# Optimization experiments

Measured on AMD Instinct MI355X. Metric: run time of the kernel, lower is better.

The kernel has to match this reference:

```python
import jax, jax.numpy as jnp
import numpy as np

B, IN_DIM, C, E, TOPK = 16384, 768, 50, 8, 2
RH = 256          # router hidden_dim
HS = [512, 256]   # expert hidden_sizes
THR = 0.05        # BitNet-1.58b ternarization threshold


def _xavier(k, shape):
    fan_out, fan_in = shape[-2], shape[-1]
    lim = float(np.sqrt(6.0 / (fan_in + fan_out)))
    return jax.random.uniform(k, shape, jnp.float32, -lim, lim)


def setup_inputs() -> dict:
    key = jax.random.key(0)
    ks = jax.random.split(key, 8)
    return {
        "x": jax.random.normal(ks[0], (B, IN_DIM), jnp.float32),
        # Router MLP: in_dim -> RH -> RH//2 -> E (torch Linear: W is (out,in))
        "rW1": _xavier(ks[1], (RH, IN_DIM)), "rb1": jnp.zeros((RH,), jnp.float32),
        "rW2": _xavier(ks[2], (RH // 2, RH)), "rb2": jnp.zeros((RH // 2,), jnp.float32),
        "rW3": _xavier(ks[3], (E, RH // 2)), "rb3": jnp.zeros((E,), jnp.float32),
        # Stacked expert weights: (E, out, in)
        "eW1": _xavier(ks[4], (E, HS[0], IN_DIM)), "eb1": jnp.zeros((E, HS[0]), jnp.float32),
        "eW2": _xavier(ks[5], (E, HS[1], HS[0])), "eb2": jnp.zeros((E, HS[1]), jnp.float32),
        "eW3": _xavier(ks[6], (E, C, HS[1])), "eb3": jnp.zeros((E, C), jnp.float32),
    }


def _ternary(W):
    # BitNet-1.58b: ternarize weights with |w|>threshold, scale by mean |W| per matrix
    scale = jnp.mean(jnp.abs(W), axis=(-2, -1), keepdims=True)
    Wq = jnp.sign(W) * (jnp.abs(W) > THR).astype(W.dtype)
    return Wq * scale


def reference(x, rW1, rb1, rW2, rb2, rW3, rb3, eW1, eb1, eW2, eb2, eW3, eb3):
    # ---- Router (eval mode: dropout = identity) ----
    h = jax.nn.relu(x @ rW1.T + rb1)
    h = jax.nn.relu(h @ rW2.T + rb2)
    router_logits = h @ rW3.T + rb3                      # (B, E)
    router_p = jax.nn.softmax(router_logits, axis=1)     # (B, E)

    # ---- Top-k gating; scatter gate weights back to dense (B, E) ----
    k_val, k_idx = jax.lax.top_k(router_p, TOPK)         # (B, K)
    rows = jnp.arange(x.shape[0])[:, None]
    gate = jnp.zeros_like(router_p).at[rows, k_idx].set(k_val)  # 0 for unselected experts

    # ---- Batched ternary-quantized expert MLPs (all experts, all samples) ----
    W1q, W2q, W3q = _ternary(eW1), _ternary(eW2), _ternary(eW3)
    a1 = jax.nn.relu(jnp.einsum('bd,ehd->ebh', x, W1q) + eb1[:, None, :])   # (E,B,H1)
    a2 = jax.nn.relu(jnp.einsum('ebh,egh->ebg', a1, W2q) + eb2[:, None, :]) # (E,B,H2)
    expert_logits = jnp.einsum('ebg,ecg->ebc', a2, W3q) + eb3[:, None, :]   # (E,B,C)

    # ---- Weighted combine over top-k experts (equivalent to the per-expert loop) ----
    out = jnp.einsum('ebc,be->bc', expert_logits, gate) / TOPK              # (B,C)

    lb_loss = jnp.float32(0.0)  # eval mode: self.training is False
    return (out, router_p, lb_loss)
```

## Files before the change

### kernel.cpp

```cpp
#include <hip/hip_runtime.h>
#include <hip/hip_bf16.h>

typedef __attribute__((ext_vector_type(4))) float f32x4;
typedef __attribute__((ext_vector_type(8))) short bf16x8;

#define B_ROWS 16384
#define IN_DIM 768
#define H1 512
#define H2 256
#define NC 50
#define NE 8
#define RH1 256
#define RH2 128
#define CHK 128
#define CHKX 64

static __device__ __forceinline__ f32x4 mfma16(bf16x8 a, bf16x8 b, f32x4 c) {
    return __builtin_amdgcn_mfma_f32_16x16x32_bf16(a, b, c, 0, 0, 0);
}

typedef __attribute__((address_space(1))) const unsigned int gas_u32;
typedef __attribute__((address_space(3))) unsigned int las_u32;
static __device__ __forceinline__ void gl16(const void* g, void* l) {
    __builtin_amdgcn_global_load_lds((gas_u32*)g, (las_u32*)l, 16, 0, 0);
}

static __device__ __forceinline__ bf16x8 expand_frag(uint2 pw) {
    unsigned q0 = (pw.x & 0x01010101u) << 7;
    unsigned q1 = (pw.y & 0x01010101u) << 7;
    union { unsigned u[4]; bf16x8 v; } r;
    r.u[0] = __builtin_amdgcn_perm(pw.x, q0, 0x05010400u);
    r.u[1] = __builtin_amdgcn_perm(pw.x, q0, 0x07030602u);
    r.u[2] = __builtin_amdgcn_perm(pw.y, q1, 0x05010400u);
    r.u[3] = __builtin_amdgcn_perm(pw.y, q1, 0x07030602u);
    return r.v;
}

static __device__ __forceinline__ void decomp_f4(float4 v, ushort4* hv, ushort4* lv) {
    float vv[4] = {v.x, v.y, v.z, v.w};
    ushort ho[4], lo4[4];
    #pragma unroll
    for (int q = 0; q < 4; ++q) {
        __hip_bfloat16 h = __float2bfloat16(vv[q]);
        float hf = __bfloat162float(h);
        __hip_bfloat16 l = __float2bfloat16(vv[q] - hf);
        ho[q] = *(ushort*)&h; lo4[q] = *(ushort*)&l;
    }
    *hv = make_ushort4(ho[0], ho[1], ho[2], ho[3]);
    *lv = make_ushort4(lo4[0], lo4[1], lo4[2], lo4[3]);
}

static __device__ __forceinline__ ushort4 cvt_f4_bf16(float4 v) {
    float vv[4] = {v.x, v.y, v.z, v.w};
    ushort ho[4];
    #pragma unroll
    for (int q = 0; q < 4; ++q) {
        __hip_bfloat16 h = __float2bfloat16(vv[q]);
        ho[q] = *(ushort*)&h;
    }
    return make_ushort4(ho[0], ho[1], ho[2], ho[3]);
}

__global__ __launch_bounds__(512) void pack_absum_kernel(
    const float* __restrict__ eW1, const float* __restrict__ eW2, const float* __restrict__ eW3,
    unsigned char* __restrict__ W1p8, unsigned char* __restrict__ W2p8,
    unsigned char* __restrict__ W3p8,
    float* __restrict__ p1, float* __restrict__ p2, float* __restrict__ p3)
{
    const int mat = blockIdx.y >> 3, e = blockIdx.y & 7;
    const int u = blockIdx.x * 512 + threadIdx.x;
    const float* src; unsigned char* dst; int valid = 1; float* P; int np;
    if (mat == 0) {
        int lane = u & 63, nblk = (u >> 6) & 31, ks = u >> 11;
        int n = nblk * 16 + (lane & 15), k = ks * 32 + (lane >> 4) * 8;
        src = eW1 + ((size_t)e * H1 + n) * IN_DIM + k;
        dst = W1p8 + (size_t)e * 393216
            + (size_t)ks * 16384 + (nblk >> 1) * 1024 + lane * 16 + (nblk & 1) * 8;
        P = p1; np = 96;
    } else if (mat == 1) {
        if (u >= 16384) return;
        int lane = u & 63, nblk = (u >> 6) & 15, ks = u >> 10;
        int n = nblk * 16 + (lane & 15), k = ks * 32 + (lane >> 4) * 8;
        src = eW2 + ((size_t)e * H2 + n) * H1 + k;
        dst = W2p8 + (size_t)e * 131072
            + (size_t)ks * 8192 + (nblk >> 1) * 1024 + lane * 16 + (nblk & 1) * 8;
        P = p2; np = 32;
    } else {
        if (u >= 2048) return;
        int lane = u & 63, nblk = (u >> 6) & 3, ks = u >> 8;
        int n = nblk * 16 + (lane & 15), k = ks * 32 + (lane >> 4) * 8;
        valid = (n < NC);
        src = eW3 + ((size_t)e * NC + (valid ? n : 0)) * H2 + k;
        dst = W3p8 + ((size_t)e * 2048 + u) * 8;
        P = p3; np = 4;
    }
    unsigned lo = 0, hi = 0;
    float s = 0.f;
    #pragma unroll
    for (int j = 0; j < 4; ++j) {
        float w = valid ? src[j] : 0.f;
        s += fabsf(w);
        unsigned c = (fabsf(w) > 0.05f) ? (w > 0.f ? 0x3Fu : 0xBFu) : 0u;
        lo |= c << (8 * j);
    }
    #pragma unroll
    for (int j = 0; j < 4; ++j) {
        float w = valid ? src[4 + j] : 0.f;
        s += fabsf(w);
        unsigned c = (fabsf(w) > 0.05f) ? (w > 0.f ? 0x3Fu : 0xBFu) : 0u;
        hi |= c << (8 * j);
    }
    *(uint2*)dst = make_uint2(lo, hi);
    const int lane = threadIdx.x & 63, wave = threadIdx.x >> 6;
    #pragma unroll
    for (int o = 32; o; o >>= 1) s += __shfl_down(s, o);
    __shared__ float red[8];
    if (lane == 0) red[wave] = s;
    __syncthreads();
    if (threadIdx.x == 0) {
        float t = 0.f;
        #pragma unroll
        for (int i = 0; i < 8; ++i) t += red[i];
        P[e * np + blockIdx.x] = t;
    }
}

__global__ __launch_bounds__(64) void finalize_scales_kernel(
    const float* __restrict__ p1, const float* __restrict__ p2, const float* __restrict__ p3,
    float* __restrict__ s1, float* __restrict__ s2, float* __restrict__ s3,
    int* __restrict__ counts)
{
    int t = threadIdx.x;
    if (t < 8) {
        float a = 0.f;
        for (int i = 0; i < 96; ++i) a += p1[t * 96 + i];
        s1[t] = a / (float)(H1 * IN_DIM);
    } else if (t < 16) {
        int e = t - 8; float a = 0.f;
        for (int i = 0; i < 32; ++i) a += p2[e * 32 + i];
        s2[e] = a / (float)(H2 * H1);
    } else if (t < 24) {
        int e = t - 16; float a = 0.f;
        for (int i = 0; i < 4; ++i) a += p3[e * 4 + i];
        s3[e] = a / (float)(NC * H2);
    } else if (t < 32) {
        counts[t - 24] = 0;
    }
}

__global__ __launch_bounds__(512) void pack_router_kernel(
    const float* __restrict__ rW1, ushort* __restrict__ rw1hp, ushort* __restrict__ rw1lp,
    const float* __restrict__ rW2, ushort* __restrict__ rw2hp, ushort* __restrict__ rw2lp)
{
    int u = blockIdx.x * 512 + threadIdx.x;
    const float* src; ushort* dh; ushort* dl;
    if (u < 24576) {
        int lane = u & 63, nblk = (u >> 6) & 15, ks = u >> 10;
        int n = nblk * 16 + (lane & 15), k = ks * 32 + (lane >> 4) * 8;
        src = rW1 + (size_t)n * IN_DIM + k;
        dh = rw1hp + (size_t)u * 8; dl = rw1lp + (size_t)u * 8;
    } else {
        int v = u - 24576;
        if (v >= 4096) return;
        int lane = v & 63, nblk = (v >> 6) & 7, ks = v >> 9;
        int n = nblk * 16 + (lane & 15), k = ks * 32 + (lane >> 4) * 8;
        src = rW2 + (size_t)n * RH1 + k;
        dh = rw2hp + (size_t)v * 8; dl = rw2lp + (size_t)v * 8;
    }
    ushort oh[8], ol[8];
    #pragma unroll
    for (int j = 0; j < 8; ++j) {
        float w = src[j];
        __hip_bfloat16 h = __float2bfloat16(w);
        float hf = __bfloat162float(h);
        __hip_bfloat16 l = __float2bfloat16(w - hf);
        oh[j] = *(ushort*)&h; ol[j] = *(ushort*)&l;
    }
    ((ushort4*)dh)[0] = make_ushort4(oh[0], oh[1], oh[2], oh[3]);
    ((ushort4*)dh)[1] = make_ushort4(oh[4], oh[5], oh[6], oh[7]);
    ((ushort4*)dl)[0] = make_ushort4(ol[0], ol[1], ol[2], ol[3]);
    ((ushort4*)dl)[1] = make_ushort4(ol[4], ol[5], ol[6], ol[7]);
}

__global__ __launch_bounds__(1024) void router_fused_kernel(
    const float* __restrict__ x,
    const ushort* __restrict__ rw1hp, const ushort* __restrict__ rw1lp, const float* __restrict__ rb1,
    const ushort* __restrict__ rw2hp, const ushort* __restrict__ rw2lp, const float* __restrict__ rb2,
    const float* __restrict__ rW3, const float* __restrict__ rb3,
    float* __restrict__ router_p, float* __restrict__ gate,
    float* __restrict__ lb_out, int* __restrict__ t2)
{
    __shared__ __align__(16) unsigned char smem[134144];
    unsigned char* Wst = smem;
    ushort (*Xdh)[32][136] = (ushort(*)[32][136])(smem + 65536);
    ushort (*Xdl)[32][136] = (ushort(*)[32][136])(smem + 65536 + 17408);
    float (*h2s)[132]      = (float(*)[132])(smem + 65536);
    ushort (*h1hs)[264]    = (ushort(*)[264])(smem + 100352);
    ushort (*h1ls)[264]    = (ushort(*)[264])(smem + 117248);

    const int tid = threadIdx.x, wave = tid >> 6, lane = tid & 63;
    const int lm = lane & 15, lk = lane >> 4;
    const int r0 = blockIdx.x * 32;

    const int srow = tid >> 5;
    const int sc4r = (tid & 31) * 4;
    const float* sg = x + (size_t)(r0 + srow) * IN_DIM + sc4r;

    float4 sv = *(const float4*)sg;
    gl16(rw1hp + tid * 8, Wst + tid * 16);
    gl16(rw1lp + tid * 8, Wst + 16384 + tid * 16);
    {
        ushort4 hv, lv;
        decomp_f4(sv, &hv, &lv);
        *(ushort4*)&Xdh[0][srow][sc4r] = hv;
        *(ushort4*)&Xdl[0][srow][sc4r] = lv;
    }
    __syncthreads();

    {
        f32x4 acc[2] = {};
        for (int s = 0; s < 24; ++s) {
            const int c = s >> 2;
            const unsigned char* curh = Wst + (s & 1) * 32768;
            const unsigned char* curl = curh + 16384;
            if (s + 1 < 24) {
                unsigned char* dst = Wst + ((s + 1) & 1) * 32768;
                gl16(rw1hp + (size_t)(s + 1) * 8192 + tid * 8, dst + tid * 16);
                gl16(rw1lp + (size_t)(s + 1) * 8192 + tid * 8, dst + 16384 + tid * 16);
            } else {
                if (tid < 512) gl16(rw2hp + tid * 8, Wst + tid * 16);
                else           gl16(rw2lp + (tid & 511) * 8, Wst + 16384 + (tid & 511) * 16);
            }
            if ((s & 3) == 0 && c < 5)
                sv = *(const float4*)(sg + (c + 1) * CHK);
            const ushort (*Xch)[136] = Xdh[c & 1];
            const ushort (*Xcl)[136] = Xdl[c & 1];
            const int ko = (s & 3) * 32 + lk * 8;
            bf16x8 ah0 = *(const bf16x8*)&Xch[lm][ko];
            bf16x8 al0 = *(const bf16x8*)&Xcl[lm][ko];
            bf16x8 ah1 = *(const bf16x8*)&Xch[16 + lm][ko];
            bf16x8 al1 = *(const bf16x8*)&Xcl[16 + lm][ko];
            bf16x8 bh = *(const bf16x8*)(curh + (wave * 64 + lane) * 16);
            bf16x8 bl = *(const bf16x8*)(curl + (wave * 64 + lane) * 16);
            acc[0] = mfma16(ah0, bh, acc[0]);
            acc[0] = mfma16(ah0, bl, acc[0]);
            acc[0] = mfma16(al0, bh, acc[0]);
            acc[1] = mfma16(ah1, bh, acc[1]);
            acc[1] = mfma16(ah1, bl, acc[1]);
            acc[1] = mfma16(al1, bh, acc[1]);
            if ((s & 3) == 2 && c < 5) {
                ushort4 hv, lv;
                decomp_f4(sv, &hv, &lv);
                *(ushort4*)&Xdh[(c + 1) & 1][srow][sc4r] = hv;
                *(ushort4*)&Xdl[(c + 1) & 1][srow][sc4r] = lv;
            }
            __syncthreads();
        }
        int col = wave * 16 + lm;
        float bv = rb1[col];
        #pragma unroll
        for (int m = 0; m < 2; ++m)
            #pragma unroll
            for (int r = 0; r < 4; ++r) {
                float v = acc[m][r] + bv;
                v = v > 0.f ? v : 0.f;
                __hip_bfloat16 h = __float2bfloat16(v);
                float hf = __bfloat162float(h);
                __hip_bfloat16 l = __float2bfloat16(v - hf);
                int row = m * 16 + lk * 4 + r;
                h1hs[row][col] = *(ushort*)&h;
                h1ls[row][col] = *(ushort*)&l;
            }
    }
    __syncthreads();

    {
        const int mt = wave >> 3, nb = wave & 7;
        f32x4 acc2 = {};
        for (int s = 0; s < 8; ++s) {
            const unsigned char* curh = Wst + (s & 1) * 32768;
            const unsigned char* curl = curh + 16384;
            if (s + 1 < 8) {
                unsigned char* dst = Wst + ((s + 1) & 1) * 32768;
                if (tid < 512) gl16(rw2hp + (size_t)(s + 1) * 4096 + tid * 8, dst + tid * 16);
                else           gl16(rw2lp + (size_t)(s + 1) * 4096 + (tid & 511) * 8, dst + 16384 + (tid & 511) * 16);
            }
            const int ko = s * 32 + lk * 8;
            bf16x8 ah = *(const bf16x8*)&h1hs[mt * 16 + lm][ko];
            bf16x8 al = *(const bf16x8*)&h1ls[mt * 16 + lm][ko];
            bf16x8 bh = *(const bf16x8*)(curh + (nb * 64 + lane) * 16);
            bf16x8 bl = *(const bf16x8*)(curl + (nb * 64 + lane) * 16);
            acc2 = mfma16(ah, bh, acc2);
            acc2 = mfma16(ah, bl, acc2);
            acc2 = mfma16(al, bh, acc2);
            __syncthreads();
        }
        int col2 = nb * 16 + lm;
        float bv = rb2[col2];
        #pragma unroll
        for (int r = 0; r < 4; ++r) {
            float v = acc2[r] + bv;
            h2s[mt * 16 + lk * 4 + r][col2] = v > 0.f ? v : 0.f;
        }
    }
    __syncthreads();

    const int o = lane >> 3, kq = lane & 7;
    #pragma unroll
    for (int i = 0; i < 2; ++i) {
        int rloc = wave * 2 + i;
        int b = r0 + rloc;
        float s = 0.f;
        #pragma unroll
        for (int q = 0; q < 4; ++q) {
            float4 hv = *(const float4*)&h2s[rloc][kq * 16 + q * 4];
            float4 wv = *(const float4*)&rW3[o * RH2 + kq * 16 + q * 4];
            s += hv.x * wv.x + hv.y * wv.y + hv.z * wv.z + hv.w * wv.w;
        }
        s += __shfl_xor(s, 1);
        s += __shfl_xor(s, 2);
        s += __shfl_xor(s, 4);
        float logit = s + rb3[o];
        float l[8];
        #pragma unroll
        for (int j = 0; j < 8; ++j) l[j] = __shfl(logit, j * 8);
        float m = l[0];
        #pragma unroll
        for (int j = 1; j < 8; ++j) m = fmaxf(m, l[j]);
        float p[8]; float sum = 0.f;
        #pragma unroll
        for (int j = 0; j < 8; ++j) { p[j] = expf(l[j] - m); sum += p[j]; }
        float inv = 1.f / sum;
        #pragma unroll
        for (int j = 0; j < 8; ++j) p[j] *= inv;
        int i1 = 0; float v1 = p[0];
        #pragma unroll
        for (int j = 1; j < 8; ++j) if (p[j] > v1) { v1 = p[j]; i1 = j; }
        int i2 = -1; float v2 = -1.f;
        #pragma unroll
        for (int j = 0; j < 8; ++j) if (j != i1 && p[j] > v2) { v2 = p[j]; i2 = j; }
        if (lane < 8) {
            router_p[(size_t)b * 8 + lane] = p[lane];
            float gv = (lane == i1) ? v1 * 0.5f : ((lane == i2) ? v2 * 0.5f : 0.f);
            gate[(size_t)b * 8 + lane] = gv;
        }
        if (lane == 0) t2[b] = i1 | (i2 << 8);
    }
    if (blockIdx.x == 0 && tid == 0) lb_out[0] = 0.f;
}

__global__ __launch_bounds__(256) void build_lists_kernel(
    const int* __restrict__ t2, int* __restrict__ counts, int* __restrict__ ent)
{
    __shared__ int hist[8], base[8];
    const int r = blockIdx.x * 256 + threadIdx.x;
    if (threadIdx.x < 8) hist[threadIdx.x] = 0;
    __syncthreads();
    const int v = t2[r];
    const int i1 = v & 255, i2 = v >> 8;
    const int rk1 = atomicAdd(&hist[i1], 1);
    const int rk2 = atomicAdd(&hist[i2], 1);
    __syncthreads();
    if (threadIdx.x < 8) base[threadIdx.x] = atomicAdd(&counts[threadIdx.x], hist[threadIdx.x]);
    __syncthreads();
    ent[i1 * B_ROWS + base[i1] + rk1] = (r << 1);
    ent[i2 * B_ROWS + base[i2] + rk2] = (r << 1) | 1;
}

__global__ __launch_bounds__(1024) void expert_fused_kernel(
    const float* __restrict__ x,
    const unsigned char* __restrict__ W1p8, const unsigned char* __restrict__ W2p8,
    const unsigned char* __restrict__ W3p8,
    const float* __restrict__ s1, const float* __restrict__ s2, const float* __restrict__ s3,
    const float* __restrict__ eb1, const float* __restrict__ eb2, const float* __restrict__ eb3,
    const float* __restrict__ gate,
    const int* __restrict__ counts, const int* __restrict__ ent,
    float* __restrict__ S0, float* __restrict__ S1)
{
    int pfx[9]; pfx[0] = 0;
    #pragma unroll
    for (int i = 0; i < 8; ++i) pfx[i + 1] = pfx[i] + ((counts[i] + 63) >> 6);
    const int T = pfx[8];
    const int R = (T + 7) >> 3;
    const int xcd = blockIdx.x & 7, j = blockIdx.x >> 3;
    if (j >= R) return;
    const int g = xcd * R + j;
    if (g >= T) return;
    int e = 0;
    #pragma unroll
    for (int i = 0; i < 7; ++i) if (g >= pfx[i + 1]) e = i + 1;
    const int t = g - pfx[e];
    const int cnt = counts[e];

    __shared__ __align__(16) unsigned char smem[151552];
    unsigned char* Wst = smem;
    __hip_bfloat16 (*A2s)[264] = (__hip_bfloat16(*)[264])(smem + 32768);
    __hip_bfloat16 (*A1s)[520] = (__hip_bfloat16(*)[520])(smem + 66560);
    ushort (*Xd)[64][72]       = (ushort(*)[64][72])(smem + 133120);
    __shared__ int rowL[64];
    __shared__ int slotL[64];
    __shared__ float gL[64];

    const int tid = threadIdx.x;
    const int wave = tid >> 6;
    const int lane = tid & 63;
    const int lm = lane & 15;
    const int lk = lane >> 4;

    if (tid < 64) {
        int idx = t * 64 + tid;
        if (idx < cnt) {
            int entv = ent[e * B_ROWS + idx];
            int r = entv >> 1;
            rowL[tid] = r;
            slotL[tid] = entv & 1;
            gL[tid] = gate[(size_t)r * NE + e];
        } else {
            rowL[tid] = -1; slotL[tid] = 0; gL[tid] = 0.f;
        }
    }
    __syncthreads();

    const int srow = tid >> 4;
    const int sc4  = (tid & 15) * 4;
    int SR = rowL[srow]; if (SR < 0) SR = 0;
    const float* sg = x + (size_t)SR * IN_DIM + sc4;
    const unsigned char* Wsrc1 = W1p8 + (size_t)e * 393216;
    const unsigned char* Wsrc2 = W2p8 + (size_t)e * 131072;
    const unsigned char* Wsrc3 = W3p8 + (size_t)e * 16384;

    float4 sv = *(const float4*)sg;
    gl16(Wsrc1 + tid * 16, Wst + tid * 16);
    gl16(Wsrc1 + 16384 + tid * 16, Wst + 16384 + tid * 16);
    *(ushort4*)&Xd[0][srow][sc4] = cvt_f4_bf16(sv);
    __syncthreads();

    {
        f32x4 acc[4][2] = {};
        const int w2 = wave * 2;
        for (int i = 0; i < 12; ++i) {
            const unsigned char* buf = Wst + (i & 1) * 32768;
            if (i + 1 < 12) {
                unsigned char* dst = Wst + ((i + 1) & 1) * 32768;
                gl16(Wsrc1 + (size_t)(i + 1) * 32768 + tid * 16, dst + tid * 16);
                gl16(Wsrc1 + (size_t)(i + 1) * 32768 + 16384 + tid * 16, dst + 16384 + tid * 16);
            } else {
                gl16(Wsrc2 + tid * 16, Wst + tid * 16);
                gl16(Wsrc2 + 16384 + tid * 16, Wst + 16384 + tid * 16);
            }
            if (i + 1 < 12) sv = *(const float4*)(sg + (i + 1) * CHKX);
            const ushort (*Xc)[72] = Xd[i & 1];
            #pragma unroll
            for (int k2 = 0; k2 < 2; ++k2) {
                const unsigned char* cur = buf + k2 * 16384;
                const int ko = k2 * 32 + lk * 8;
                bf16x8 a0 = *(const bf16x8*)&Xc[     lm][ko];
                bf16x8 a1 = *(const bf16x8*)&Xc[16 + lm][ko];
                bf16x8 a2 = *(const bf16x8*)&Xc[32 + lm][ko];
                bf16x8 a3 = *(const bf16x8*)&Xc[48 + lm][ko];
                uint4 pw4 = *(const uint4*)(cur + wave * 1024 + lane * 16);
                bf16x8 b0 = expand_frag(make_uint2(pw4.x, pw4.y));
                bf16x8 b1 = expand_frag(make_uint2(pw4.z, pw4.w));
                acc[0][0] = mfma16(a0, b0, acc[0][0]);
                acc[1][0] = mfma16(a1, b0, acc[1][0]);
                acc[2][0] = mfma16(a2, b0, acc[2][0]);
                acc[3][0] = mfma16(a3, b0, acc[3][0]);
                acc[0][1] = mfma16(a0, b1, acc[0][1]);
                acc[1][1] = mfma16(a1, b1, acc[1][1]);
                acc[2][1] = mfma16(a2, b1, acc[2][1]);
                acc[3][1] = mfma16(a3, b1, acc[3][1]);
            }
            if (i + 1 < 12) *(ushort4*)&Xd[(i + 1) & 1][srow][sc4] = cvt_f4_bf16(sv);
            __syncthreads();
        }
        const float* bias = eb1 + e * H1;
        const float sc = s1[e];
        #pragma unroll
        for (int n = 0; n < 2; ++n) {
            int ncol = (w2 + n) * 16 + lm;
            float bv = bias[ncol];
            #pragma unroll
            for (int m = 0; m < 4; ++m)
                #pragma unroll
                for (int r = 0; r < 4; ++r) {
                    float v = fmaf(acc[m][n][r], sc, bv);
                    v = v > 0.f ? v : 0.f;
                    A1s[m * 16 + lk * 4 + r][ncol] = __float2bfloat16(v);
                }
        }
    }
    __syncthreads();

    {
        const int mt = wave >> 3, ntw = wave & 7;
        f32x4 acc[2][2] = {};
        for (int i = 0; i < 4; ++i) {
            const unsigned char* buf = Wst + (i & 1) * 32768;
            if (i + 1 < 4) {
                unsigned char* dst = Wst + ((i + 1) & 1) * 32768;
                gl16(Wsrc2 + (size_t)(i + 1) * 32768 + tid * 16, dst + tid * 16);
                gl16(Wsrc2 + (size_t)(i + 1) * 32768 + 16384 + tid * 16, dst + 16384 + tid * 16);
            } else {
                gl16(Wsrc3 + tid * 16, Wst + tid * 16);
            }
            #pragma unroll
            for (int k4 = 0; k4 < 4; ++k4) {
                const unsigned char* cur = buf + k4 * 8192;
                const int s = i * 4 + k4;
                const int ko = s * 32 + lk * 8;
                bf16x8 a0 = *(const bf16x8*)&A1s[mt * 32 +      lm][ko];
                bf16x8 a1 = *(const bf16x8*)&A1s[mt * 32 + 16 + lm][ko];
                uint4 pw4 = *(const uint4*)(cur + ntw * 1024 + lane * 16);
                bf16x8 b0 = expand_frag(make_uint2(pw4.x, pw4.y));
                bf16x8 b1 = expand_frag(make_uint2(pw4.z, pw4.w));
                acc[0][0] = mfma16(a0, b0, acc[0][0]);
                acc[1][0] = mfma16(a1, b0, acc[1][0]);
                acc[0][1] = mfma16(a0, b1, acc[0][1]);
                acc[1][1] = mfma16(a1, b1, acc[1][1]);
            }
            __syncthreads();
        }
        const float* bias = eb2 + e * H2;
        const float sc = s2[e];
        #pragma unroll
        for (int n = 0; n < 2; ++n) {
            int ncol = (ntw * 2 + n) * 16 + lm;
            float bv = bias[ncol];
            #pragma unroll
            for (int m = 0; m < 2; ++m)
                #pragma unroll
                for (int r = 0; r < 4; ++r) {
                    float v = fmaf(acc[m][n][r], sc, bv);
                    v = v > 0.f ? v : 0.f;
                    A2s[mt * 32 + m * 16 + lk * 4 + r][ncol] = __float2bfloat16(v);
                }
        }
    }
    __syncthreads();

    {
        const int mt = wave & 3, nt = wave >> 2;
        f32x4 acc = {};
        #pragma unroll
        for (int s = 0; s < 8; ++s) {
            bf16x8 a = *(const bf16x8*)&A2s[mt * 16 + lm][s * 32 + lk * 8];
            uint2 pw = *(const uint2*)(Wst + ((s * 4 + nt) * 64 + lane) * 8);
            bf16x8 b = expand_frag(pw);
            acc = mfma16(a, b, acc);
        }
        int col = nt * 16 + lm;
        if (col < NC) {
            const float bv = eb3[e * NC + col];
            const float sc = s3[e];
            #pragma unroll
            for (int r = 0; r < 4; ++r) {
                int row = mt * 16 + lk * 4 + r;
                int R2 = rowL[row];
                if (R2 >= 0) {
                    float v = gL[row] * fmaf(acc[r], sc, bv);
                    float* Sb = slotL[row] ? S1 : S0;
                    Sb[(size_t)R2 * 64 + col] = v;
                }
            }
        }
    }
}

__global__ __launch_bounds__(256) void combine_kernel(
    const float* __restrict__ S0, const float* __restrict__ S1, float* __restrict__ out)
{
    int i = blockIdx.x * 256 + threadIdx.x;
    if (i < B_ROWS * NC) {
        int row = i / NC, col = i % NC;
        out[i] = S0[(size_t)row * 64 + col] + S1[(size_t)row * 64 + col];
    }
}

extern "C" void kernel_launch(void* const* d_in, const int* in_sizes, int n_in,
                              void* d_out, int out_size, void* d_ws, size_t ws_size,
                              hipStream_t stream) {
    const float* x   = (const float*)d_in[0];
    const float* rW1 = (const float*)d_in[1];
    const float* rb1 = (const float*)d_in[2];
    const float* rW2 = (const float*)d_in[3];
    const float* rb2 = (const float*)d_in[4];
    const float* rW3 = (const float*)d_in[5];
    const float* rb3 = (const float*)d_in[6];
    const float* eW1 = (const float*)d_in[7];
    const float* eb1 = (const float*)d_in[8];
    const float* eW2 = (const float*)d_in[9];
    const float* eb2 = (const float*)d_in[10];
    const float* eW3 = (const float*)d_in[11];
    const float* eb3 = (const float*)d_in[12];

    float* out_main = (float*)d_out;
    float* router_p = out_main + (size_t)B_ROWS * NC;
    float* lb_out   = router_p + (size_t)B_ROWS * NE;

    char* ws = (char*)d_ws;
    size_t off = 0;
    unsigned char* W1p8 = (unsigned char*)(ws + off); off += (size_t)NE * 49152 * 8;
    unsigned char* W2p8 = (unsigned char*)(ws + off); off += (size_t)NE * 16384 * 8;
    unsigned char* W3p8 = (unsigned char*)(ws + off); off += (size_t)NE * 2048 * 8;
    float* S0   = (float*)(ws + off);  off += (size_t)B_ROWS * 64 * 4;
    float* S1   = (float*)(ws + off);  off += (size_t)B_ROWS * 64 * 4;
    ushort* rw1hp = (ushort*)(ws + off); off += (size_t)24576 * 8 * 2;
    ushort* rw1lp = (ushort*)(ws + off); off += (size_t)24576 * 8 * 2;
    ushort* rw2hp = (ushort*)(ws + off); off += (size_t)4096 * 8 * 2;
    ushort* rw2lp = (ushort*)(ws + off); off += (size_t)4096 * 8 * 2;
    float* gate = (float*)(ws + off);  off += (size_t)B_ROWS * NE * 4;
    int*   ent  = (int*)(ws + off);    off += (size_t)NE * B_ROWS * 4;
    int*   t2   = (int*)(ws + off);    off += (size_t)B_ROWS * 4;
    int* counts = (int*)(ws + off);    off += 256;
    float* s1   = (float*)(ws + off);  off += 256;
    float* s2   = (float*)(ws + off);  off += 256;
    float* s3   = (float*)(ws + off);  off += 256;
    float* p1   = (float*)(ws + off);  off += NE * 96 * 4;
    float* p2   = (float*)(ws + off);  off += NE * 32 * 4;
    float* p3   = (float*)(ws + off);  off += NE * 4 * 4;

    pack_absum_kernel<<<dim3(96, 24), 512, 0, stream>>>(
        eW1, eW2, eW3, W1p8, W2p8, W3p8, p1, p2, p3);
    pack_router_kernel<<<56, 512, 0, stream>>>(rW1, rw1hp, rw1lp, rW2, rw2hp, rw2lp);
    finalize_scales_kernel<<<1, 64, 0, stream>>>(p1, p2, p3, s1, s2, s3, counts);

    router_fused_kernel<<<B_ROWS / 32, 1024, 0, stream>>>(
        x, rw1hp, rw1lp, rb1, rw2hp, rw2lp, rb2, rW3, rb3, router_p, gate, lb_out, t2);
    build_lists_kernel<<<B_ROWS / 256, 256, 0, stream>>>(t2, counts, ent);

    expert_fused_kernel<<<1024, 1024, 0, stream>>>(
        x, W1p8, W2p8, W3p8, s1, s2, s3, eb1, eb2, eb3, gate, counts, ent, S0, S1);
    combine_kernel<<<(B_ROWS * NC + 255) / 256, 256, 0, stream>>>(S0, S1, out_main);
}
```

Measured before the change: 145.4 us.

## Load packed ternary weights directly into registers instead of staging through LDS

Drops the global_load_lds double-buffered weight staging in all three expert layers. Each wave now reads its own packed weight fragments straight from global memory into registers, prefetched one step ahead. The X chunk grows to 128 columns, which halves the layer-1 iterations and barriers, and layer 2 loses its per-step barriers. LDS use falls from about 148KB to about 99KB, which may allow more resident blocks, at the cost of more VGPRs and exposed global-load latency that the LDS path used to hide.

```diff
diff --git a/kernel.cpp b/kernel.cpp
--- a/kernel.cpp
+++ b/kernel.cpp
@@ -13,7 +13,6 @@
 #define RH1 256
 #define RH2 128
 #define CHK 128
-#define CHKX 64
 
 static __device__ __forceinline__ f32x4 mfma16(bf16x8 a, bf16x8 b, f32x4 c) {
     return __builtin_amdgcn_mfma_f32_16x16x32_bf16(a, b, c, 0, 0, 0);
@@ -392,11 +391,10 @@
     const int t = g - pfx[e];
     const int cnt = counts[e];
 
-    __shared__ __align__(16) unsigned char smem[151552];
-    unsigned char* Wst = smem;
-    __hip_bfloat16 (*A2s)[264] = (__hip_bfloat16(*)[264])(smem + 32768);
-    __hip_bfloat16 (*A1s)[520] = (__hip_bfloat16(*)[520])(smem + 66560);
-    ushort (*Xd)[64][72]       = (ushort(*)[64][72])(smem + 133120);
+    __shared__ __align__(16) unsigned char smem[101376];
+    __hip_bfloat16 (*A1s)[520] = (__hip_bfloat16(*)[520])(smem);
+    __hip_bfloat16 (*A2s)[264] = (__hip_bfloat16(*)[264])(smem + 66560);
+    ushort (*Xd)[64][136]      = (ushort(*)[64][136])(smem + 66560);
     __shared__ int rowL[64];
     __shared__ int slotL[64];
     __shared__ float gL[64];
@@ -422,45 +420,53 @@
     __syncthreads();
 
     const int srow = tid >> 4;
-    const int sc4  = (tid & 15) * 4;
+    const int sc8  = (tid & 15) * 8;
     int SR = rowL[srow]; if (SR < 0) SR = 0;
-    const float* sg = x + (size_t)SR * IN_DIM + sc4;
+    const float* sg = x + (size_t)SR * IN_DIM + sc8;
     const unsigned char* Wsrc1 = W1p8 + (size_t)e * 393216;
     const unsigned char* Wsrc2 = W2p8 + (size_t)e * 131072;
     const unsigned char* Wsrc3 = W3p8 + (size_t)e * 16384;
 
-    float4 sv = *(const float4*)sg;
-    gl16(Wsrc1 + tid * 16, Wst + tid * 16);
-    gl16(Wsrc1 + 16384 + tid * 16, Wst + 16384 + tid * 16);
-    *(ushort4*)&Xd[0][srow][sc4] = cvt_f4_bf16(sv);
+    {
+        float4 fa = *(const float4*)(sg);
+        float4 fb = *(const float4*)(sg + 4);
+        *(ushort4*)&Xd[0][srow][sc8]     = cvt_f4_bf16(fa);
+        *(ushort4*)&Xd[0][srow][sc8 + 4] = cvt_f4_bf16(fb);
+    }
     __syncthreads();
 
     {
         f32x4 acc[4][2] = {};
         const int w2 = wave * 2;
-        for (int i = 0; i < 12; ++i) {
-            const unsigned char* buf = Wst + (i & 1) * 32768;
-            if (i + 1 < 12) {
-                unsigned char* dst = Wst + ((i + 1) & 1) * 32768;
-                gl16(Wsrc1 + (size_t)(i + 1) * 32768 + tid * 16, dst + tid * 16);
-                gl16(Wsrc1 + (size_t)(i + 1) * 32768 + 16384 + tid * 16, dst + 16384 + tid * 16);
-            } else {
-                gl16(Wsrc2 + tid * 16, Wst + tid * 16);
-                gl16(Wsrc2 + 16384 + tid * 16, Wst + 16384 + tid * 16);
-            }
-            if (i + 1 < 12) sv = *(const float4*)(sg + (i + 1) * CHKX);
-            const ushort (*Xc)[72] = Xd[i & 1];
+        const unsigned char* wp1 = Wsrc1 + wave * 1024 + lane * 16;
+        uint4 pw[4];
+        #pragma unroll
+        for (int k = 0; k < 4; ++k)
+            pw[k] = *(const uint4*)(wp1 + (size_t)k * 16384);
+        for (int i = 0; i < 6; ++i) {
+            float4 fa, fb;
+            if (i + 1 < 6) {
+                fa = *(const float4*)(sg + (i + 1) * CHK);
+                fb = *(const float4*)(sg + (i + 1) * CHK + 4);
+            }
+            uint4 cur[4];
             #pragma unroll
-            for (int k2 = 0; k2 < 2; ++k2) {
-                const unsigned char* cur = buf + k2 * 16384;
-                const int ko = k2 * 32 + lk * 8;
+            for (int k = 0; k < 4; ++k) cur[k] = pw[k];
+            if (i + 1 < 6) {
+                #pragma unroll
+                for (int k = 0; k < 4; ++k)
+                    pw[k] = *(const uint4*)(wp1 + (size_t)(4 * i + 4 + k) * 16384);
+            }
+            const ushort (*Xc)[136] = Xd[i & 1];
+            #pragma unroll
+            for (int k4 = 0; k4 < 4; ++k4) {
+                const int ko = k4 * 32 + lk * 8;
                 bf16x8 a0 = *(const bf16x8*)&Xc[     lm][ko];
                 bf16x8 a1 = *(const bf16x8*)&Xc[16 + lm][ko];
                 bf16x8 a2 = *(const bf16x8*)&Xc[32 + lm][ko];
                 bf16x8 a3 = *(const bf16x8*)&Xc[48 + lm][ko];
-                uint4 pw4 = *(const uint4*)(cur + wave * 1024 + lane * 16);
-                bf16x8 b0 = expand_frag(make_uint2(pw4.x, pw4.y));
-                bf16x8 b1 = expand_frag(make_uint2(pw4.z, pw4.w));
+                bf16x8 b0 = expand_frag(make_uint2(cur[k4].x, cur[k4].y));
+                bf16x8 b1 = expand_frag(make_uint2(cur[k4].z, cur[k4].w));
                 acc[0][0] = mfma16(a0, b0, acc[0][0]);
                 acc[1][0] = mfma16(a1, b0, acc[1][0]);
                 acc[2][0] = mfma16(a2, b0, acc[2][0]);
@@ -470,7 +476,10 @@
                 acc[2][1] = mfma16(a2, b1, acc[2][1]);
                 acc[3][1] = mfma16(a3, b1, acc[3][1]);
             }
-            if (i + 1 < 12) *(ushort4*)&Xd[(i + 1) & 1][srow][sc4] = cvt_f4_bf16(sv);
+            if (i + 1 < 6) {
+                *(ushort4*)&Xd[(i + 1) & 1][srow][sc8]     = cvt_f4_bf16(fa);
+                *(ushort4*)&Xd[(i + 1) & 1][srow][sc8 + 4] = cvt_f4_bf16(fb);
+            }
             __syncthreads();
         }
         const float* bias = eb1 + e * H1;
@@ -493,32 +502,38 @@
 
     {
         const int mt = wave >> 3, ntw = wave & 7;
+        const unsigned char* wp2 = Wsrc2 + ntw * 1024 + lane * 16;
         f32x4 acc[2][2] = {};
-        for (int i = 0; i < 4; ++i) {
-            const unsigned char* buf = Wst + (i & 1) * 32768;
-            if (i + 1 < 4) {
-                unsigned char* dst = Wst + ((i + 1) & 1) * 32768;
-                gl16(Wsrc2 + (size_t)(i + 1) * 32768 + tid * 16, dst + tid * 16);
-                gl16(Wsrc2 + (size_t)(i + 1) * 32768 + 16384 + tid * 16, dst + 16384 + tid * 16);
-            } else {
-                gl16(Wsrc3 + tid * 16, Wst + tid * 16);
-            }
-            #pragma unroll
-            for (int k4 = 0; k4 < 4; ++k4) {
-                const unsigned char* cur = buf + k4 * 8192;
-                const int s = i * 4 + k4;
+        uint4 pwa = *(const uint4*)(wp2);
+        uint4 pwb = *(const uint4*)(wp2 + 8192);
+        for (int s = 0; s < 16; s += 2) {
+            uint4 c0 = pwa, c1 = pwb;
+            if (s + 2 < 16) {
+                pwa = *(const uint4*)(wp2 + (size_t)(s + 2) * 8192);
+                pwb = *(const uint4*)(wp2 + (size_t)(s + 3) * 8192);
+            }
+            {
                 const int ko = s * 32 + lk * 8;
                 bf16x8 a0 = *(const bf16x8*)&A1s[mt * 32 +      lm][ko];
                 bf16x8 a1 = *(const bf16x8*)&A1s[mt * 32 + 16 + lm][ko];
-                uint4 pw4 = *(const uint4*)(cur + ntw * 1024 + lane * 16);
-                bf16x8 b0 = expand_frag(make_uint2(pw4.x, pw4.y));
-                bf16x8 b1 = expand_frag(make_uint2(pw4.z, pw4.w));
+                bf16x8 b0 = expand_frag(make_uint2(c0.x, c0.y));
+                bf16x8 b1 = expand_frag(make_uint2(c0.z, c0.w));
                 acc[0][0] = mfma16(a0, b0, acc[0][0]);
                 acc[1][0] = mfma16(a1, b0, acc[1][0]);
                 acc[0][1] = mfma16(a0, b1, acc[0][1]);
                 acc[1][1] = mfma16(a1, b1, acc[1][1]);
             }
-            __syncthreads();
+            {
+                const int ko = (s + 1) * 32 + lk * 8;
+                bf16x8 a0 = *(const bf16x8*)&A1s[mt * 32 +      lm][ko];
+                bf16x8 a1 = *(const bf16x8*)&A1s[mt * 32 + 16 + lm][ko];
+                bf16x8 b0 = expand_frag(make_uint2(c1.x, c1.y));
+                bf16x8 b1 = expand_frag(make_uint2(c1.z, c1.w));
+                acc[0][0] = mfma16(a0, b0, acc[0][0]);
+                acc[1][0] = mfma16(a1, b0, acc[1][0]);
+                acc[0][1] = mfma16(a0, b1, acc[0][1]);
+                acc[1][1] = mfma16(a1, b1, acc[1][1]);
+            }
         }
         const float* bias = eb2 + e * H2;
         const float sc = s2[e];
@@ -544,7 +559,7 @@
         #pragma unroll
         for (int s = 0; s < 8; ++s) {
             bf16x8 a = *(const bf16x8*)&A2s[mt * 16 + lm][s * 32 + lk * 8];
-            uint2 pw = *(const uint2*)(Wst + ((s * 4 + nt) * 64 + lane) * 8);
+            uint2 pw = *(const uint2*)(Wsrc3 + ((s * 4 + nt) * 64 + lane) * 8);
             bf16x8 b = expand_frag(pw);
             acc = mfma16(a, b, acc);
         }
```

New measurement: 140.6 us. 3.3% less time.
